# Kernel optimization log

Measured on AMD Instinct MI355X. Metric: run time of the kernel, lower is better.

Reference implementation:

```python
import jax, jax.numpy as jnp
import numpy as np

# Model dims (match init_kwargs)
B, N, COORD, F0 = 16, 512, 3, 64
K = 8            # kernels per layer
F1, F2 = 128, 256  # conv filters
POOL = 2
FC = 512
EPS = 1e-9


def _pairwise(C):
    """Pairwise euclidean distances D [B,N,N] and direction cosines Cos [B,N,N] from coords C [B,N,3]."""
    dot = jnp.einsum('bic,bjc->bij', C, C)
    l2 = jnp.einsum('bic,bic->bi', C, C)
    d2 = l2[:, :, None] + l2[:, None, :] - 2.0 * dot
    D = jnp.sqrt(jnp.abs(d2) + EPS)
    nrm = jnp.sqrt(l2 + EPS)
    Cos = dot / (nrm[:, :, None] * nrm[:, None, :])
    return D, Cos


def _layer(V, D, Cos, gkw, gkb, acw, acb, gcw, gcb, bng, bnb):
    """GraphKernels -> AngularContribution -> GraphConv -> tanh -> batchnorm (eval)."""
    b, n, f = V.shape
    # GraphKernels: node-dependent learned Gaussian decay over pairwise distances
    u = jax.nn.softplus(V @ gkw + gkb)                # [B,N,K]
    uk = jnp.transpose(u, (0, 2, 1))[..., None]       # [B,K,N,1]
    A = jnp.exp(-(D[:, None] ** 2) * uk)              # [B,K,N,N]
    # AngularContribution: learned interpolation between isotropic and cosine-weighted kernel
    w = jax.nn.sigmoid(V @ acw + acb)                 # [B,N,K]
    wk = jnp.transpose(w, (0, 2, 1))[..., None]       # [B,K,N,1]
    A = A * (wk * Cos[:, None] + (1.0 - wk))          # [B,K,N,N]
    # GraphConv: per-kernel message passing then shared dense over [self || messages]
    M = jnp.einsum('bkij,bjf->bikf', A, V).reshape(b, n, -1)  # [B,N,K*F]
    H = jnp.concatenate([V, M], axis=-1) @ gcw + gcb           # [B,N,F_out]
    H = jnp.tanh(H)
    # batchnorm in eval mode (moving mean 0, var 1): affine only
    return bng * H + bnb


def _pool(V, C, p):
    """AverageSeqGraphPool: average consecutive (sequence-ordered) nodes with window/stride p."""
    b, n, f = V.shape
    return V.reshape(b, n // p, p, f).mean(2), C.reshape(b, n // p, p, -1).mean(2)


def setup_inputs() -> dict:
    key = jax.random.key(0)
    ks = jax.random.split(key, 12)
    def w(k, shape):
        return jax.random.normal(k, shape, jnp.float32) / np.sqrt(shape[0])
    flat_dim = (N // POOL // POOL) * F2
    return {
        'V': jax.random.normal(ks[0], (B, N, F0), jnp.float32),
        'C': jax.random.normal(ks[1], (B, N, COORD), jnp.float32) * 10.0,  # ~Angstrom-scale coords
        'gk_w0': w(ks[2], (F0, K)), 'gk_b0': jnp.zeros((K,), jnp.float32),
        'ac_w0': w(ks[3], (F0, K)), 'ac_b0': jnp.zeros((K,), jnp.float32),
        'gc_w0': w(ks[4], ((K + 1) * F0, F1)), 'gc_b0': jnp.zeros((F1,), jnp.float32),
        'bn_g0': jnp.ones((F1,), jnp.float32), 'bn_b0': jnp.zeros((F1,), jnp.float32),
        'gk_w1': w(ks[5], (F1, K)), 'gk_b1': jnp.zeros((K,), jnp.float32),
        'ac_w1': w(ks[6], (F1, K)), 'ac_b1': jnp.zeros((K,), jnp.float32),
        'gc_w1': w(ks[7], ((K + 1) * F1, F2)), 'gc_b1': jnp.zeros((F2,), jnp.float32),
        'bn_g1': jnp.ones((F2,), jnp.float32), 'bn_b1': jnp.zeros((F2,), jnp.float32),
        'fc_w': w(ks[8], (flat_dim, FC)), 'fc_b': jnp.zeros((FC,), jnp.float32),
    }


def reference(V, C, gk_w0, gk_b0, ac_w0, ac_b0, gc_w0, gc_b0, bn_g0, bn_b0,
              gk_w1, gk_b1, ac_w1, ac_b1, gc_w1, gc_b1, bn_g1, bn_b1, fc_w, fc_b):
    D, Cos = _pairwise(C)
    H = _layer(V, D, Cos, gk_w0, gk_b0, ac_w0, ac_b0, gc_w0, gc_b0, bn_g0, bn_b0)
    H, C1 = _pool(H, C, POOL)
    D, Cos = _pairwise(C1)
    H = _layer(H, D, Cos, gk_w1, gk_b1, ac_w1, ac_b1, gc_w1, gc_b1, bn_g1, bn_b1)
    H, _ = _pool(H, C1, POOL)
    Flat = H.reshape(H.shape[0], -1)  # [B, 128*256]
    return jax.nn.sigmoid(Flat @ fc_w + fc_b)  # [B, 512]
```

## Files before the change

kernel.cpp:

```cpp
#include <hip/hip_runtime.h>
#include <math.h>

#define KK 8
#define EPSF 1e-9f

typedef unsigned int   uint32;
typedef unsigned short u16;
typedef __attribute__((ext_vector_type(8))) short bf16x8;
typedef __attribute__((ext_vector_type(4))) float f32x4;

#define MFMA_16x16x32(a, b, c) __builtin_amdgcn_mfma_f32_16x16x32_bf16(a, b, c, 0, 0, 0)

typedef __attribute__((address_space(1))) const unsigned int glob_cu32;
typedef __attribute__((address_space(3))) unsigned int lds_u32;
__device__ __forceinline__ void g2l16(const void* gsrc, void* ldst) {
    __builtin_amdgcn_global_load_lds((glob_cu32*)gsrc, (lds_u32*)ldst, 16, 0, 0);
}

__device__ __forceinline__ int swz(int row, int o) {
    return (row << 6) + (((o) ^ (row & 7)) << 3);
}

__device__ __forceinline__ float softplusf(float x) {
    return x > 0.0f ? x + log1pf(expf(-x)) : log1pf(expf(x));
}
__device__ __forceinline__ float sigmoidf_(float x) {
    return 1.0f / (1.0f + expf(-x));
}
__device__ __forceinline__ u16 f2bf(float f) {
    union { float f; uint32 u; } v; v.f = f;
    uint32 u = v.u;
    return (u16)((u + 0x7FFFu + ((u >> 16) & 1u)) >> 16);
}

__global__ __launch_bounds__(256)
void prep_kernel(const float* __restrict__ V, const float* __restrict__ W0,
                 const float* __restrict__ W1, u16* __restrict__ VT0,
                 u16* __restrict__ Wt0, u16* __restrict__ Wt1) {
    __shared__ float s[64][65];
    int blk = blockIdx.x, tid = threadIdx.x;
    if (blk < 128) {
        int b = blk >> 3, rt = blk & 7;
#pragma unroll
        for (int t = 0; t < 16; t++) {
            int idx = t * 256 + tid; int r = idx >> 6, c = idx & 63;
            s[r][c] = V[((size_t)b * 512 + rt * 64 + r) * 64 + c];
        }
        __syncthreads();
#pragma unroll
        for (int t = 0; t < 16; t++) {
            int idx = t * 256 + tid; int f = idx >> 6, j = idx & 63;
            VT0[((size_t)b * 64 + f) * 512 + rt * 64 + j] = f2bf(s[j][f]);
        }
    } else if (blk < 146) {
        int t0 = blk - 128; int rt = t0 >> 1, ct = t0 & 1;
#pragma unroll
        for (int t = 0; t < 16; t++) {
            int idx = t * 256 + tid; int r = idx >> 6, c = idx & 63;
            s[r][c] = W0[((size_t)rt * 64 + r) * 128 + ct * 64 + c];
        }
        __syncthreads();
#pragma unroll
        for (int t = 0; t < 16; t++) {
            int idx = t * 256 + tid; int f = idx >> 6, j = idx & 63;
            Wt0[((size_t)ct * 64 + f) * 576 + rt * 64 + j] = f2bf(s[j][f]);
        }
    } else {
        int t0 = blk - 146; int rt = t0 >> 2, ct = t0 & 3;
#pragma unroll
        for (int t = 0; t < 16; t++) {
            int idx = t * 256 + tid; int r = idx >> 6, c = idx & 63;
            s[r][c] = W1[((size_t)rt * 64 + r) * 256 + ct * 64 + c];
        }
        __syncthreads();
#pragma unroll
        for (int t = 0; t < 16; t++) {
            int idx = t * 256 + tid; int f = idx >> 6, j = idx & 63;
            Wt1[((size_t)ct * 64 + f) * 1152 + rt * 64 + j] = f2bf(s[j][f]);
        }
    }
}

__global__ __launch_bounds__(256)
void layer0_fused(const u16* __restrict__ VT0, const float* __restrict__ C,
                  const float* __restrict__ V,
                  const float* __restrict__ gw, const float* __restrict__ gb,
                  const float* __restrict__ aw, const float* __restrict__ ab,
                  const u16* __restrict__ Wt0, const float* __restrict__ bias,
                  const float* __restrict__ bng, const float* __restrict__ bnb,
                  float* __restrict__ H0p, u16* __restrict__ VT1) {
    int b = blockIdx.x >> 5, tile = blockIdx.x & 31;
    int i0 = tile * 16;
    int tid = threadIdx.x;
    int wv = tid >> 6, lane = tid & 63, quad = lane >> 4, l15 = lane & 15;

    __shared__ __align__(16) u16 s_mem[12288];
    __shared__ __align__(16) u16 s_X[16 * 584];
    __shared__ __align__(16) float s_ci[16][4];
    __shared__ float s_u[16][KK];
    __shared__ float s_w[16][KK];

    u16* s_vT = s_mem;
    u16* s_A  = s_mem + 4096;
    u16* s_W  = s_mem;

    {
        int t = tid & 127;
        int i = t >> 3, k = t & 7;
        const float4* xr = (const float4*)(V + ((size_t)b * 512 + i0 + i) * 64);
        const float* wm = (tid < 128) ? gw : aw;
        float s = 0.f;
#pragma unroll
        for (int f4 = 0; f4 < 16; f4++) {
            float4 x = xr[f4];
            s += x.x * wm[(f4 * 4 + 0) * 8 + k] + x.y * wm[(f4 * 4 + 1) * 8 + k]
               + x.z * wm[(f4 * 4 + 2) * 8 + k] + x.w * wm[(f4 * 4 + 3) * 8 + k];
        }
        if (tid < 128) s_u[i][k] = softplusf(s + gb[k]);
        else           s_w[i][k] = sigmoidf_(s + ab[k]);
    }
    if (tid < 16) {
        const float* cp = C + ((size_t)b * 512 + i0 + tid) * 3;
        float x = cp[0], y = cp[1], z = cp[2];
        s_ci[tid][0] = x; s_ci[tid][1] = y; s_ci[tid][2] = z;
        s_ci[tid][3] = x * x + y * y + z * z;
    }
    {
        int row = tid >> 4, f4 = tid & 15;
        float4 x = *(const float4*)(V + ((size_t)b * 512 + i0 + row) * 64 + f4 * 4);
        *(uint32*)&s_X[row * 584 + f4 * 4]     = (uint32)f2bf(x.x) | ((uint32)f2bf(x.y) << 16);
        *(uint32*)&s_X[row * 584 + f4 * 4 + 2] = (uint32)f2bf(x.z) | ((uint32)f2bf(x.w) << 16);
    }

    f32x4 acc[2][4] = {};
    for (int j0 = 0; j0 < 512; j0 += 64) {
        const float* cp = C + ((size_t)b * 512 + j0 + lane) * 3;
        float cjx = cp[0], cjy = cp[1], cjz = cp[2];
        float l2j = cjx * cjx + cjy * cjy + cjz * cjz;
        __syncthreads();
#pragma unroll
        for (int p = 0; p < 2; p++) {
            int s = p * 256 + wv * 64 + lane;
            int f = s >> 3, op = s & 7;
            g2l16(VT0 + ((size_t)b * 64 + f) * 512 + j0 + ((op ^ (f & 7)) << 3),
                  (void*)(s_vT + (p * 256 + wv * 64) * 8));
        }
#pragma unroll
        for (int t = 0; t < 4; t++) {
            int i = t * 4 + wv, j = lane;
            float dot = s_ci[i][0] * cjx + s_ci[i][1] * cjy + s_ci[i][2] * cjz;
            float d2 = fabsf(s_ci[i][3] + l2j - 2.f * dot) + EPSF;
            float cs = dot / sqrtf((s_ci[i][3] + EPSF) * (l2j + EPSF));
            f32x4 u01 = *(const f32x4*)&s_u[i][0];
            f32x4 u23 = *(const f32x4*)&s_u[i][4];
            f32x4 w01 = *(const f32x4*)&s_w[i][0];
            f32x4 w23 = *(const f32x4*)&s_w[i][4];
#pragma unroll
            for (int k = 0; k < 4; k++) {
                float a = __expf(-d2 * u01[k]) * (w01[k] * cs + 1.f - w01[k]);
                int row = i * 8 + k;
                s_A[(row << 6) + (((j >> 3) ^ (row & 7)) << 3) + (j & 7)] = f2bf(a);
            }
#pragma unroll
            for (int k = 0; k < 4; k++) {
                float a = __expf(-d2 * u23[k]) * (w23[k] * cs + 1.f - w23[k]);
                int row = i * 8 + 4 + k;
                s_A[(row << 6) + (((j >> 3) ^ (row & 7)) << 3) + (j & 7)] = f2bf(a);
            }
        }
        __syncthreads();
#pragma unroll
        for (int ks = 0; ks < 2; ks++) {
            int o = ks * 4 + quad;
            bf16x8 a0 = *(const bf16x8*)&s_A[swz(wv * 32 + l15, o)];
            bf16x8 a1 = *(const bf16x8*)&s_A[swz(wv * 32 + 16 + l15, o)];
#pragma unroll
            for (int cf = 0; cf < 4; cf++) {
                bf16x8 bv = *(const bf16x8*)&s_vT[swz(cf * 16 + l15, o)];
                acc[0][cf] = MFMA_16x16x32(a0, bv, acc[0][cf]);
                acc[1][cf] = MFMA_16x16x32(a1, bv, acc[1][cf]);
            }
        }
    }

#pragma unroll
    for (int rf = 0; rf < 2; rf++)
#pragma unroll
        for (int cf = 0; cf < 4; cf++)
#pragma unroll
            for (int r = 0; r < 4; r++) {
                int arow = wv * 32 + rf * 16 + quad * 4 + r;
                int i = arow >> 3, k = arow & 7;
                s_X[i * 584 + 64 + k * 64 + cf * 16 + l15] = f2bf(acc[rf][cf][r]);
            }

    f32x4 acc2[2] = {};
    for (int kc = 0; kc < 576; kc += 64) {
        __syncthreads();
#pragma unroll
        for (int p = 0; p < 4; p++) {
            int s = p * 256 + wv * 64 + lane;
            int c = s >> 3, op = s & 7;
            g2l16(Wt0 + (size_t)c * 576 + kc + ((op ^ (c & 7)) << 3),
                  (void*)(s_W + (p * 256 + wv * 64) * 8));
        }
        __syncthreads();
#pragma unroll
        for (int ks = 0; ks < 2; ks++) {
            int o = ks * 4 + quad;
            bf16x8 av = *(const bf16x8*)&s_X[l15 * 584 + kc + o * 8];
#pragma unroll
            for (int cf = 0; cf < 2; cf++) {
                bf16x8 bv = *(const bf16x8*)&s_W[swz(wv * 32 + cf * 16 + l15, o)];
                acc2[cf] = MFMA_16x16x32(av, bv, acc2[cf]);
            }
        }
    }

#pragma unroll
    for (int cf = 0; cf < 2; cf++) {
        int col = wv * 32 + cf * 16 + l15;
        float bs = bias[col], gg = bng[col], bb = bnb[col];
        float h0 = gg * tanhf(acc2[cf][0] + bs) + bb;
        float h1 = gg * tanhf(acc2[cf][1] + bs) + bb;
        float h2 = gg * tanhf(acc2[cf][2] + bs) + bb;
        float h3 = gg * tanhf(acc2[cf][3] + bs) + bb;
        float p0 = 0.5f * (h0 + h1), p1 = 0.5f * (h2 + h3);
        int pl = tile * 8 + quad * 2;
        H0p[((size_t)b * 256 + pl) * 128 + col] = p0;
        H0p[((size_t)b * 256 + pl + 1) * 128 + col] = p1;
        VT1[((size_t)b * 128 + col) * 256 + pl]     = f2bf(p0);
        VT1[((size_t)b * 128 + col) * 256 + pl + 1] = f2bf(p1);
    }
}

__global__ __launch_bounds__(256)
void layer1_fused(const u16* __restrict__ VT1, const float* __restrict__ C,
                  const float* __restrict__ H0p,
                  const float* __restrict__ gw, const float* __restrict__ gb,
                  const float* __restrict__ aw, const float* __restrict__ ab,
                  const u16* __restrict__ Wt1, const float* __restrict__ bias,
                  const float* __restrict__ bng, const float* __restrict__ bnb,
                  float* __restrict__ H1p) {
    int b = blockIdx.x >> 5, tile = blockIdx.x & 31;
    int i0 = tile * 8;
    int tid = threadIdx.x;
    int wv = tid >> 6, lane = tid & 63, quad = lane >> 4, l15 = lane & 15;

    __shared__ __align__(16) u16 s_mem[16384];
    __shared__ __align__(16) u16 s_X1[8 * 1160];
    __shared__ __align__(16) float s_ci[8][4];
    __shared__ float s_u[8][KK];
    __shared__ float s_w[8][KK];

    u16* s_vT = s_mem;
    u16* s_A  = s_mem + 8192;
    u16* s_W  = s_mem;

    if (wv < 2) {
        int t = tid & 63;
        int i = t >> 3, k = t & 7;
        const float4* xr = (const float4*)(H0p + ((size_t)b * 256 + i0 + i) * 128);
        const float* wm = (wv == 0) ? gw : aw;
        float s = 0.f;
#pragma unroll
        for (int f4 = 0; f4 < 32; f4++) {
            float4 x = xr[f4];
            s += x.x * wm[(f4 * 4 + 0) * 8 + k] + x.y * wm[(f4 * 4 + 1) * 8 + k]
               + x.z * wm[(f4 * 4 + 2) * 8 + k] + x.w * wm[(f4 * 4 + 3) * 8 + k];
        }
        if (wv == 0) s_u[i][k] = softplusf(s + gb[k]);
        else         s_w[i][k] = sigmoidf_(s + ab[k]);
    }
    if (tid < 8) {
        const float* cp = C + ((size_t)b * 512 + 2 * (i0 + tid)) * 3;
        float x = 0.5f * (cp[0] + cp[3]);
        float y = 0.5f * (cp[1] + cp[4]);
        float z = 0.5f * (cp[2] + cp[5]);
        s_ci[tid][0] = x; s_ci[tid][1] = y; s_ci[tid][2] = z;
        s_ci[tid][3] = x * x + y * y + z * z;
    }
    {
        int row = tid >> 5, f4 = tid & 31;
        float4 x = *(const float4*)(H0p + ((size_t)b * 256 + i0 + row) * 128 + f4 * 4);
        *(uint32*)&s_X1[row * 1160 + f4 * 4]     = (uint32)f2bf(x.x) | ((uint32)f2bf(x.y) << 16);
        *(uint32*)&s_X1[row * 1160 + f4 * 4 + 2] = (uint32)f2bf(x.z) | ((uint32)f2bf(x.w) << 16);
    }

    f32x4 acc[8] = {};
    for (int j0 = 0; j0 < 256; j0 += 64) {
        const float* cp = C + ((size_t)b * 512 + 2 * (j0 + lane)) * 3;
        float cjx = 0.5f * (cp[0] + cp[3]);
        float cjy = 0.5f * (cp[1] + cp[4]);
        float cjz = 0.5f * (cp[2] + cp[5]);
        float l2j = cjx * cjx + cjy * cjy + cjz * cjz;
        __syncthreads();
#pragma unroll
        for (int p = 0; p < 4; p++) {
            int s = p * 256 + wv * 64 + lane;
            int f = s >> 3, op = s & 7;
            g2l16(VT1 + ((size_t)b * 128 + f) * 256 + j0 + ((op ^ (f & 7)) << 3),
                  (void*)(s_vT + (p * 256 + wv * 64) * 8));
        }
#pragma unroll
        for (int t = 0; t < 2; t++) {
            int i = t * 4 + wv, j = lane;
            float dot = s_ci[i][0] * cjx + s_ci[i][1] * cjy + s_ci[i][2] * cjz;
            float d2 = fabsf(s_ci[i][3] + l2j - 2.f * dot) + EPSF;
            float cs = dot / sqrtf((s_ci[i][3] + EPSF) * (l2j + EPSF));
            f32x4 u01 = *(const f32x4*)&s_u[i][0];
            f32x4 u23 = *(const f32x4*)&s_u[i][4];
            f32x4 w01 = *(const f32x4*)&s_w[i][0];
            f32x4 w23 = *(const f32x4*)&s_w[i][4];
#pragma unroll
            for (int k = 0; k < 4; k++) {
                float a = __expf(-d2 * u01[k]) * (w01[k] * cs + 1.f - w01[k]);
                int row = i * 8 + k;
                s_A[(row << 6) + (((j >> 3) ^ (row & 7)) << 3) + (j & 7)] = f2bf(a);
            }
#pragma unroll
            for (int k = 0; k < 4; k++) {
                float a = __expf(-d2 * u23[k]) * (w23[k] * cs + 1.f - w23[k]);
                int row = i * 8 + 4 + k;
                s_A[(row << 6) + (((j >> 3) ^ (row & 7)) << 3) + (j & 7)] = f2bf(a);
            }
        }
        __syncthreads();
#pragma unroll
        for (int ks = 0; ks < 2; ks++) {
            int o = ks * 4 + quad;
            bf16x8 a0 = *(const bf16x8*)&s_A[swz(wv * 16 + l15, o)];
#pragma unroll
            for (int cf = 0; cf < 8; cf++) {
                bf16x8 bv = *(const bf16x8*)&s_vT[swz(cf * 16 + l15, o)];
                acc[cf] = MFMA_16x16x32(a0, bv, acc[cf]);
            }
        }
    }

#pragma unroll
    for (int cf = 0; cf < 8; cf++)
#pragma unroll
        for (int r = 0; r < 4; r++) {
            int arow = wv * 16 + quad * 4 + r;
            int i = arow >> 3, k = arow & 7;
            s_X1[i * 1160 + 128 + k * 128 + cf * 16 + l15] = f2bf(acc[cf][r]);
        }

    f32x4 acc2[4] = {};
    for (int kc = 0; kc < 1152; kc += 64) {
        __syncthreads();
#pragma unroll
        for (int p = 0; p < 8; p++) {
            int s = p * 256 + wv * 64 + lane;
            int c = s >> 3, op = s & 7;
            g2l16(Wt1 + (size_t)c * 1152 + kc + ((op ^ (c & 7)) << 3),
                  (void*)(s_W + (p * 256 + wv * 64) * 8));
        }
        __syncthreads();
#pragma unroll
        for (int ks = 0; ks < 2; ks++) {
            int o = ks * 4 + quad;
            bf16x8 av = *(const bf16x8*)&s_X1[(l15 & 7) * 1160 + kc + o * 8];
#pragma unroll
            for (int cf = 0; cf < 4; cf++) {
                bf16x8 bv = *(const bf16x8*)&s_W[swz(wv * 64 + cf * 16 + l15, o)];
                acc2[cf] = MFMA_16x16x32(av, bv, acc2[cf]);
            }
        }
    }

#pragma unroll
    for (int cf = 0; cf < 4; cf++) {
        int col = wv * 64 + cf * 16 + l15;
        float bs = bias[col], gg = bng[col], bb = bnb[col];
        float h0 = gg * tanhf(acc2[cf][0] + bs) + bb;
        float h1 = gg * tanhf(acc2[cf][1] + bs) + bb;
        float h2 = gg * tanhf(acc2[cf][2] + bs) + bb;
        float h3 = gg * tanhf(acc2[cf][3] + bs) + bb;
        if (quad < 2) {
            float p0 = 0.5f * (h0 + h1), p1 = 0.5f * (h2 + h3);
            int pl = tile * 4 + quad * 2;
            H1p[((size_t)b * 128 + pl) * 256 + col] = p0;
            H1p[((size_t)b * 128 + pl + 1) * 256 + col] = p1;
        }
    }
}

__global__ __launch_bounds__(256)
void fc_partial_kernel(const float* __restrict__ Flat, const float* __restrict__ W,
                       float* __restrict__ P) {
    int cs = blockIdx.x & 3, ks = blockIdx.x >> 2;
    int m0 = ks * 256;
    int c4 = threadIdx.x & 31;
    int msub = threadIdx.x >> 5;

    __shared__ __align__(16) float xT[256][16];

#pragma unroll
    for (int q = 0; q < 16; q++) {
        int idx = q * 256 + threadIdx.x;
        int b = idx >> 8, mm = idx & 255;
        int bg = (b >> 2) ^ (mm & 3);
        xT[mm][(bg << 2) + (b & 3)] = Flat[(size_t)b * 32768 + m0 + mm];
    }
    __syncthreads();

    const float4* W4 = (const float4*)W;
    float4 acc[16] = {};

    for (int h = 0; h < 4; h++) {
        float4 wbuf[8];
#pragma unroll
        for (int i = 0; i < 8; i++) {
            int mm = msub * 32 + h * 8 + i;
            wbuf[i] = W4[(size_t)(m0 + mm) * 128 + cs * 32 + c4];
        }
#pragma unroll
        for (int i = 0; i < 8; i++) {
            int mm = msub * 32 + h * 8 + i;
#pragma unroll
            for (int bg = 0; bg < 4; bg++) {
                float4 xv = *(const float4*)&xT[mm][((bg ^ (mm & 3)) << 2)];
                acc[bg * 4 + 0].x += xv.x * wbuf[i].x; acc[bg * 4 + 0].y += xv.x * wbuf[i].y;
                acc[bg * 4 + 0].z += xv.x * wbuf[i].z; acc[bg * 4 + 0].w += xv.x * wbuf[i].w;
                acc[bg * 4 + 1].x += xv.y * wbuf[i].x; acc[bg * 4 + 1].y += xv.y * wbuf[i].y;
                acc[bg * 4 + 1].z += xv.y * wbuf[i].z; acc[bg * 4 + 1].w += xv.y * wbuf[i].w;
                acc[bg * 4 + 2].x += xv.z * wbuf[i].x; acc[bg * 4 + 2].y += xv.z * wbuf[i].y;
                acc[bg * 4 + 2].z += xv.z * wbuf[i].z; acc[bg * 4 + 2].w += xv.z * wbuf[i].w;
                acc[bg * 4 + 3].x += xv.w * wbuf[i].x; acc[bg * 4 + 3].y += xv.w * wbuf[i].y;
                acc[bg * 4 + 3].z += xv.w * wbuf[i].z; acc[bg * 4 + 3].w += xv.w * wbuf[i].w;
            }
        }
    }
    __syncthreads();
    __shared__ __align__(16) float red[8][32][4];
#pragma unroll
    for (int b = 0; b < 16; b++) {
        red[msub][c4][0] = acc[b].x; red[msub][c4][1] = acc[b].y;
        red[msub][c4][2] = acc[b].z; red[msub][c4][3] = acc[b].w;
        __syncthreads();
        if (msub == 0) {
            float4 s = make_float4(0.f, 0.f, 0.f, 0.f);
#pragma unroll
            for (int m = 0; m < 8; m++) {
                s.x += red[m][c4][0]; s.y += red[m][c4][1];
                s.z += red[m][c4][2]; s.w += red[m][c4][3];
            }
            *(float4*)&P[((size_t)ks * 16 + b) * 512 + cs * 128 + c4 * 4] = s;
        }
        __syncthreads();
    }
}

__global__ void fc_reduce_kernel(const float* __restrict__ P, const float* __restrict__ fcb,
                                 float* __restrict__ out) {
    int idx = blockIdx.x * 256 + threadIdx.x;
    float s0 = 0.f, s1 = 0.f;
#pragma unroll 8
    for (int ks = 0; ks < 128; ks += 2) {
        s0 += P[(size_t)ks * 8192 + idx];
        s1 += P[(size_t)(ks + 1) * 8192 + idx];
    }
    float s = s0 + s1 + fcb[idx & 511];
    out[idx] = 1.f / (1.f + expf(-s));
}

extern "C" void kernel_launch(void* const* d_in, const int* in_sizes, int n_in,
                              void* d_out, int out_size, void* d_ws, size_t ws_size,
                              hipStream_t stream) {
    const float* V     = (const float*)d_in[0];
    const float* C     = (const float*)d_in[1];
    const float* gk_w0 = (const float*)d_in[2];
    const float* gk_b0 = (const float*)d_in[3];
    const float* ac_w0 = (const float*)d_in[4];
    const float* ac_b0 = (const float*)d_in[5];
    const float* gc_w0 = (const float*)d_in[6];
    const float* gc_b0 = (const float*)d_in[7];
    const float* bn_g0 = (const float*)d_in[8];
    const float* bn_b0 = (const float*)d_in[9];
    const float* gk_w1 = (const float*)d_in[10];
    const float* gk_b1 = (const float*)d_in[11];
    const float* ac_w1 = (const float*)d_in[12];
    const float* ac_b1 = (const float*)d_in[13];
    const float* gc_w1 = (const float*)d_in[14];
    const float* gc_b1 = (const float*)d_in[15];
    const float* bn_g1 = (const float*)d_in[16];
    const float* bn_b1 = (const float*)d_in[17];
    const float* fc_w  = (const float*)d_in[18];
    const float* fc_b  = (const float*)d_in[19];
    float* out = (float*)d_out;

    float* H0p = (float*)d_ws;
    float* H1p = H0p + 524288;
    float* P   = H1p + 524288;
    u16* VT0 = (u16*)(P + 1048576);
    u16* VT1 = VT0 + 524288;
    u16* Wt0 = VT1 + 524288;
    u16* Wt1 = Wt0 + 73728;

    prep_kernel<<<218, 256, 0, stream>>>(V, gc_w0, gc_w1, VT0, Wt0, Wt1);
    layer0_fused<<<512, 256, 0, stream>>>(VT0, C, V, gk_w0, gk_b0, ac_w0, ac_b0,
                                          Wt0, gc_b0, bn_g0, bn_b0, H0p, VT1);
    layer1_fused<<<512, 256, 0, stream>>>(VT1, C, H0p, gk_w1, gk_b1, ac_w1, ac_b1,
                                          Wt1, gc_b1, bn_g1, bn_b1, H1p);
    fc_partial_kernel<<<512, 256, 0, stream>>>(H1p, fc_w, P);
    fc_reduce_kernel<<<32, 256, 0, stream>>>(P, fc_b, out);
}
```

Baseline: 215.3 us.

## Vectorize adjacency generation, read GraphConv weights directly, widen fc reduction

The adjacency build is remapped so each thread handles four neighbour columns. It loads coordinates with float4, computes the per-pair distance and cosine once, and reuses them across all kernels. It writes packed bf16 pairs with 64-bit LDS stores instead of scalar 16-bit stores. The GraphConv dense step no longer stages weight tiles into LDS behind two barriers per chunk; it reads bf16 weights straight from global/L2 into MFMA operands. The layer-1 LDS buffer shrinks accordingly, which may raise occupancy. The fc reduction is split across 256 blocks with an in-block tree sum, for more parallelism on the tail kernel. The risk is that the direct weight reads are uncoalesced, strided 16-byte loads, and their L2 latency may not be hidden as well as the LDS staging did.

```diff
diff --git a/kernel.cpp b/kernel.cpp
--- a/kernel.cpp
+++ b/kernel.cpp
@@ -31,6 +31,9 @@
     union { float f; uint32 u; } v; v.f = f;
     uint32 u = v.u;
     return (u16)((u + 0x7FFFu + ((u >> 16) & 1u)) >> 16);
+}
+__device__ __forceinline__ uint32 pack2(float a, float b) {
+    return (uint32)f2bf(a) | ((uint32)f2bf(b) << 16);
 }
 
 __global__ __launch_bounds__(256)
@@ -102,7 +105,6 @@
 
     u16* s_vT = s_mem;
     u16* s_A  = s_mem + 4096;
-    u16* s_W  = s_mem;
 
     {
         int t = tid & 127;
@@ -128,15 +130,20 @@
     {
         int row = tid >> 4, f4 = tid & 15;
         float4 x = *(const float4*)(V + ((size_t)b * 512 + i0 + row) * 64 + f4 * 4);
-        *(uint32*)&s_X[row * 584 + f4 * 4]     = (uint32)f2bf(x.x) | ((uint32)f2bf(x.y) << 16);
-        *(uint32*)&s_X[row * 584 + f4 * 4 + 2] = (uint32)f2bf(x.z) | ((uint32)f2bf(x.w) << 16);
-    }
+        *(uint32*)&s_X[row * 584 + f4 * 4]     = pack2(x.x, x.y);
+        *(uint32*)&s_X[row * 584 + f4 * 4 + 2] = pack2(x.z, x.w);
+    }
+
+    int ia = tid >> 4, jg = tid & 15;
+    int oct = jg >> 1, half = (jg & 1) << 2;
 
     f32x4 acc[2][4] = {};
     for (int j0 = 0; j0 < 512; j0 += 64) {
-        const float* cp = C + ((size_t)b * 512 + j0 + lane) * 3;
-        float cjx = cp[0], cjy = cp[1], cjz = cp[2];
-        float l2j = cjx * cjx + cjy * cjy + cjz * cjz;
+        const float4* cp4 = (const float4*)(C + ((size_t)b * 512 + j0 + jg * 4) * 3);
+        float4 q0 = cp4[0], q1 = cp4[1], q2 = cp4[2];
+        float jx[4] = {q0.x, q0.w, q1.z, q2.y};
+        float jy[4] = {q0.y, q1.x, q1.w, q2.z};
+        float jz[4] = {q0.z, q1.y, q2.x, q2.w};
         __syncthreads();
 #pragma unroll
         for (int p = 0; p < 2; p++) {
@@ -145,27 +152,28 @@
             g2l16(VT0 + ((size_t)b * 64 + f) * 512 + j0 + ((op ^ (f & 7)) << 3),
                   (void*)(s_vT + (p * 256 + wv * 64) * 8));
         }
-#pragma unroll
-        for (int t = 0; t < 4; t++) {
-            int i = t * 4 + wv, j = lane;
-            float dot = s_ci[i][0] * cjx + s_ci[i][1] * cjy + s_ci[i][2] * cjz;
-            float d2 = fabsf(s_ci[i][3] + l2j - 2.f * dot) + EPSF;
-            float cs = dot / sqrtf((s_ci[i][3] + EPSF) * (l2j + EPSF));
-            f32x4 u01 = *(const f32x4*)&s_u[i][0];
-            f32x4 u23 = *(const f32x4*)&s_u[i][4];
-            f32x4 w01 = *(const f32x4*)&s_w[i][0];
-            f32x4 w23 = *(const f32x4*)&s_w[i][4];
-#pragma unroll
-            for (int k = 0; k < 4; k++) {
-                float a = __expf(-d2 * u01[k]) * (w01[k] * cs + 1.f - w01[k]);
-                int row = i * 8 + k;
-                s_A[(row << 6) + (((j >> 3) ^ (row & 7)) << 3) + (j & 7)] = f2bf(a);
-            }
-#pragma unroll
-            for (int k = 0; k < 4; k++) {
-                float a = __expf(-d2 * u23[k]) * (w23[k] * cs + 1.f - w23[k]);
-                int row = i * 8 + 4 + k;
-                s_A[(row << 6) + (((j >> 3) ^ (row & 7)) << 3) + (j & 7)] = f2bf(a);
+        {
+            float cix = s_ci[ia][0], ciy = s_ci[ia][1], ciz = s_ci[ia][2], l2i = s_ci[ia][3];
+            float d2a[4], csa[4];
+#pragma unroll
+            for (int jj = 0; jj < 4; jj++) {
+                float l2j = jx[jj] * jx[jj] + jy[jj] * jy[jj] + jz[jj] * jz[jj];
+                float dot = cix * jx[jj] + ciy * jy[jj] + ciz * jz[jj];
+                d2a[jj] = fabsf(l2i + l2j - 2.f * dot) + EPSF;
+                csa[jj] = dot / sqrtf((l2i + EPSF) * (l2j + EPSF));
+            }
+            const float* up = &s_u[ia][0];
+            const float* wp = &s_w[ia][0];
+#pragma unroll
+            for (int k = 0; k < 8; k++) {
+                float uu = up[k], ww = wp[k], om = 1.f - ww;
+                float a0 = __expf(-d2a[0] * uu) * (ww * csa[0] + om);
+                float a1 = __expf(-d2a[1] * uu) * (ww * csa[1] + om);
+                float a2 = __expf(-d2a[2] * uu) * (ww * csa[2] + om);
+                float a3 = __expf(-d2a[3] * uu) * (ww * csa[3] + om);
+                int row = ia * 8 + k;
+                uint2 pk = make_uint2(pack2(a0, a1), pack2(a2, a3));
+                *(uint2*)&s_A[(row << 6) + ((oct ^ (row & 7)) << 3) + half] = pk;
             }
         }
         __syncthreads();
@@ -193,25 +201,19 @@
                 int i = arow >> 3, k = arow & 7;
                 s_X[i * 584 + 64 + k * 64 + cf * 16 + l15] = f2bf(acc[rf][cf][r]);
             }
+    __syncthreads();
 
     f32x4 acc2[2] = {};
+#pragma unroll 3
     for (int kc = 0; kc < 576; kc += 64) {
-        __syncthreads();
-#pragma unroll
-        for (int p = 0; p < 4; p++) {
-            int s = p * 256 + wv * 64 + lane;
-            int c = s >> 3, op = s & 7;
-            g2l16(Wt0 + (size_t)c * 576 + kc + ((op ^ (c & 7)) << 3),
-                  (void*)(s_W + (p * 256 + wv * 64) * 8));
-        }
-        __syncthreads();
 #pragma unroll
         for (int ks = 0; ks < 2; ks++) {
             int o = ks * 4 + quad;
             bf16x8 av = *(const bf16x8*)&s_X[l15 * 584 + kc + o * 8];
 #pragma unroll
             for (int cf = 0; cf < 2; cf++) {
-                bf16x8 bv = *(const bf16x8*)&s_W[swz(wv * 32 + cf * 16 + l15, o)];
+                int col = wv * 32 + cf * 16 + l15;
+                bf16x8 bv = *(const bf16x8*)&Wt0[(size_t)col * 576 + kc + o * 8];
                 acc2[cf] = MFMA_16x16x32(av, bv, acc2[cf]);
             }
         }
@@ -247,7 +249,7 @@
     int tid = threadIdx.x;
     int wv = tid >> 6, lane = tid & 63, quad = lane >> 4, l15 = lane & 15;
 
-    __shared__ __align__(16) u16 s_mem[16384];
+    __shared__ __align__(16) u16 s_mem[12288];
     __shared__ __align__(16) u16 s_X1[8 * 1160];
     __shared__ __align__(16) float s_ci[8][4];
     __shared__ float s_u[8][KK];
@@ -255,7 +257,6 @@
 
     u16* s_vT = s_mem;
     u16* s_A  = s_mem + 8192;
-    u16* s_W  = s_mem;
 
     if (wv < 2) {
         int t = tid & 63;
@@ -283,17 +284,26 @@
     {
         int row = tid >> 5, f4 = tid & 31;
         float4 x = *(const float4*)(H0p + ((size_t)b * 256 + i0 + row) * 128 + f4 * 4);
-        *(uint32*)&s_X1[row * 1160 + f4 * 4]     = (uint32)f2bf(x.x) | ((uint32)f2bf(x.y) << 16);
-        *(uint32*)&s_X1[row * 1160 + f4 * 4 + 2] = (uint32)f2bf(x.z) | ((uint32)f2bf(x.w) << 16);
-    }
+        *(uint32*)&s_X1[row * 1160 + f4 * 4]     = pack2(x.x, x.y);
+        *(uint32*)&s_X1[row * 1160 + f4 * 4 + 2] = pack2(x.z, x.w);
+    }
+
+    int kh = tid >> 7, ia = (tid >> 4) & 7, jg = tid & 15;
+    int oct = jg >> 1, half = (jg & 1) << 2;
 
     f32x4 acc[8] = {};
     for (int j0 = 0; j0 < 256; j0 += 64) {
-        const float* cp = C + ((size_t)b * 512 + 2 * (j0 + lane)) * 3;
-        float cjx = 0.5f * (cp[0] + cp[3]);
-        float cjy = 0.5f * (cp[1] + cp[4]);
-        float cjz = 0.5f * (cp[2] + cp[5]);
-        float l2j = cjx * cjx + cjy * cjy + cjz * cjz;
+        const float4* cp4 = (const float4*)(C + ((size_t)b * 512 + 2 * (j0 + jg * 4)) * 3);
+        float4 q0 = cp4[0], q1 = cp4[1], q2 = cp4[2], q3 = cp4[3], q4 = cp4[4], q5 = cp4[5];
+        float r[24] = {q0.x,q0.y,q0.z,q0.w, q1.x,q1.y,q1.z,q1.w, q2.x,q2.y,q2.z,q2.w,
+                       q3.x,q3.y,q3.z,q3.w, q4.x,q4.y,q4.z,q4.w, q5.x,q5.y,q5.z,q5.w};
+        float jx[4], jy[4], jz[4];
+#pragma unroll
+        for (int jj = 0; jj < 4; jj++) {
+            jx[jj] = 0.5f * (r[6 * jj] + r[6 * jj + 3]);
+            jy[jj] = 0.5f * (r[6 * jj + 1] + r[6 * jj + 4]);
+            jz[jj] = 0.5f * (r[6 * jj + 2] + r[6 * jj + 5]);
+        }
         __syncthreads();
 #pragma unroll
         for (int p = 0; p < 4; p++) {
@@ -302,27 +312,28 @@
             g2l16(VT1 + ((size_t)b * 128 + f) * 256 + j0 + ((op ^ (f & 7)) << 3),
                   (void*)(s_vT + (p * 256 + wv * 64) * 8));
         }
-#pragma unroll
-        for (int t = 0; t < 2; t++) {
-            int i = t * 4 + wv, j = lane;
-            float dot = s_ci[i][0] * cjx + s_ci[i][1] * cjy + s_ci[i][2] * cjz;
-            float d2 = fabsf(s_ci[i][3] + l2j - 2.f * dot) + EPSF;
-            float cs = dot / sqrtf((s_ci[i][3] + EPSF) * (l2j + EPSF));
-            f32x4 u01 = *(const f32x4*)&s_u[i][0];
-            f32x4 u23 = *(const f32x4*)&s_u[i][4];
-            f32x4 w01 = *(const f32x4*)&s_w[i][0];
-            f32x4 w23 = *(const f32x4*)&s_w[i][4];
-#pragma unroll
-            for (int k = 0; k < 4; k++) {
-                float a = __expf(-d2 * u01[k]) * (w01[k] * cs + 1.f - w01[k]);
-                int row = i * 8 + k;
-                s_A[(row << 6) + (((j >> 3) ^ (row & 7)) << 3) + (j & 7)] = f2bf(a);
-            }
-#pragma unroll
-            for (int k = 0; k < 4; k++) {
-                float a = __expf(-d2 * u23[k]) * (w23[k] * cs + 1.f - w23[k]);
-                int row = i * 8 + 4 + k;
-                s_A[(row << 6) + (((j >> 3) ^ (row & 7)) << 3) + (j & 7)] = f2bf(a);
+        {
+            float cix = s_ci[ia][0], ciy = s_ci[ia][1], ciz = s_ci[ia][2], l2i = s_ci[ia][3];
+            float d2a[4], csa[4];
+#pragma unroll
+            for (int jj = 0; jj < 4; jj++) {
+                float l2j = jx[jj] * jx[jj] + jy[jj] * jy[jj] + jz[jj] * jz[jj];
+                float dot = cix * jx[jj] + ciy * jy[jj] + ciz * jz[jj];
+                d2a[jj] = fabsf(l2i + l2j - 2.f * dot) + EPSF;
+                csa[jj] = dot / sqrtf((l2i + EPSF) * (l2j + EPSF));
+            }
+            const float* up = &s_u[ia][kh * 4];
+            const float* wp = &s_w[ia][kh * 4];
+#pragma unroll
+            for (int kk = 0; kk < 4; kk++) {
+                float uu = up[kk], ww = wp[kk], om = 1.f - ww;
+                float a0 = __expf(-d2a[0] * uu) * (ww * csa[0] + om);
+                float a1 = __expf(-d2a[1] * uu) * (ww * csa[1] + om);
+                float a2 = __expf(-d2a[2] * uu) * (ww * csa[2] + om);
+                float a3 = __expf(-d2a[3] * uu) * (ww * csa[3] + om);
+                int row = ia * 8 + kh * 4 + kk;
+                uint2 pk = make_uint2(pack2(a0, a1), pack2(a2, a3));
+                *(uint2*)&s_A[(row << 6) + ((oct ^ (row & 7)) << 3) + half] = pk;
             }
         }
         __syncthreads();
@@ -346,25 +357,19 @@
             int i = arow >> 3, k = arow & 7;
             s_X1[i * 1160 + 128 + k * 128 + cf * 16 + l15] = f2bf(acc[cf][r]);
         }
+    __syncthreads();
 
     f32x4 acc2[4] = {};
+#pragma unroll 2
     for (int kc = 0; kc < 1152; kc += 64) {
-        __syncthreads();
-#pragma unroll
-        for (int p = 0; p < 8; p++) {
-            int s = p * 256 + wv * 64 + lane;
-            int c = s >> 3, op = s & 7;
-            g2l16(Wt1 + (size_t)c * 1152 + kc + ((op ^ (c & 7)) << 3),
-                  (void*)(s_W + (p * 256 + wv * 64) * 8));
-        }
-        __syncthreads();
 #pragma unroll
         for (int ks = 0; ks < 2; ks++) {
             int o = ks * 4 + quad;
             bf16x8 av = *(const bf16x8*)&s_X1[(l15 & 7) * 1160 + kc + o * 8];
 #pragma unroll
             for (int cf = 0; cf < 4; cf++) {
-                bf16x8 bv = *(const bf16x8*)&s_W[swz(wv * 64 + cf * 16 + l15, o)];
+                int col = wv * 64 + cf * 16 + l15;
+                bf16x8 bv = *(const bf16x8*)&Wt1[(size_t)col * 1152 + kc + o * 8];
                 acc2[cf] = MFMA_16x16x32(av, bv, acc2[cf]);
             }
         }
@@ -453,17 +458,23 @@
     }
 }
 
-__global__ void fc_reduce_kernel(const float* __restrict__ P, const float* __restrict__ fcb,
-                                 float* __restrict__ out) {
-    int idx = blockIdx.x * 256 + threadIdx.x;
-    float s0 = 0.f, s1 = 0.f;
-#pragma unroll 8
-    for (int ks = 0; ks < 128; ks += 2) {
-        s0 += P[(size_t)ks * 8192 + idx];
-        s1 += P[(size_t)(ks + 1) * 8192 + idx];
-    }
-    float s = s0 + s1 + fcb[idx & 511];
-    out[idx] = 1.f / (1.f + expf(-s));
+__global__ __launch_bounds__(256)
+void fc_reduce_kernel(const float* __restrict__ P, const float* __restrict__ fcb,
+                      float* __restrict__ out) {
+    __shared__ float red[8][33];
+    int o = blockIdx.x * 32 + (threadIdx.x & 31);
+    int kg = threadIdx.x >> 5;
+    float s = 0.f;
+#pragma unroll
+    for (int q = 0; q < 16; q++) s += P[(size_t)(kg * 16 + q) * 8192 + o];
+    red[kg][threadIdx.x & 31] = s;
+    __syncthreads();
+    if (kg == 0) {
+        float t = fcb[o & 511];
+#pragma unroll
+        for (int m = 0; m < 8; m++) t += red[m][threadIdx.x & 31];
+        out[o] = 1.f / (1.f + expf(-t));
+    }
 }
 
 extern "C" void kernel_launch(void* const* d_in, const int* in_sizes, int n_in,
@@ -505,5 +516,5 @@
     layer1_fused<<<512, 256, 0, stream>>>(VT1, C, H0p, gk_w1, gk_b1, ac_w1, ac_b1,
                                           Wt1, gc_b1, bn_g1, bn_b1, H1p);
     fc_partial_kernel<<<512, 256, 0, stream>>>(H1p, fc_w, P);
-    fc_reduce_kernel<<<32, 256, 0, stream>>>(P, fc_b, out);
-}
+    fc_reduce_kernel<<<256, 256, 0, stream>>>(P, fc_b, out);
+}
```

New measurement: 219.8 us. 2.1% more time.
